# Optimization experiments

Hardware: AMD Instinct MI355X
Metric: run time of the kernel (lower is better)

## Reference

```python
import jax, jax.numpy as jnp
import numpy as np

N, D, O, H, T, S, R, BN = 4096, 256, 256, 256, 512, 8, 4, 2  # nodes, in, out, hidden, text_len, adj_size, relations used, basis_num


def setup_inputs() -> dict:
    key = jax.random.key(0)
    ks = jax.random.split(key, 16)
    sc = 0.05
    return {
        "entity_embeddings": jax.random.normal(ks[0], (N, D), jnp.float32) * sc,
        "text_encodings": jax.random.normal(ks[1], (1, T, 2 * H), jnp.float32) * sc,
        "adj_to_use": jnp.arange(R, dtype=jnp.int32),
        "adj_masks": jax.random.randint(ks[2], (R, N, N), 0, 2, dtype=jnp.int32),
        "text_guids": jax.random.normal(ks[3], (S, 2 * H), jnp.float32) * sc,
        "graph_guids_1": jax.random.normal(ks[4], (S, D), jnp.float32) * sc,
        "graph_guids_2": jax.random.normal(ks[5], (S, D), jnp.float32) * sc,
        "guid_a": jax.random.normal(ks[6], (S,), jnp.float32),
        "basis_V": jax.random.normal(ks[7], (D, BN, O), jnp.float32) * sc,
        "basis_b": jax.random.normal(ks[8], (S, BN), jnp.float32) * sc,
        "W_1": jax.random.normal(ks[9], (2 * H, D), jnp.float32) * sc,
        "W_2": jax.random.normal(ks[10], (2 * H, D), jnp.float32) * sc,
        "ln_gamma": jnp.ones((O,), jnp.float32),
        "ln_beta": jnp.zeros((O,), jnp.float32),
    }


def reference(entity_embeddings, text_encodings, adj_to_use, adj_masks,
              text_guids, graph_guids_1, graph_guids_2, guid_a,
              basis_V, basis_b, W_1, W_2, ln_gamma, ln_beta):
    te = text_encodings[0]                                  # [T, 2H] (batch of 1)
    tg = text_guids[adj_to_use]                             # [R, 2H]
    # text attention: softmax over T, per relation
    att = jax.nn.softmax(te @ tg.T, axis=0)                 # [T, R]
    context = att.T @ te                                    # [R, 2H]
    c1 = context @ W_1                                      # [R, D]
    c2 = context @ W_2
    ga = jax.nn.sigmoid(guid_a[adj_to_use])[:, None]        # [R, 1]
    g1 = ga * graph_guids_1[adj_to_use] + (1.0 - ga) * c1   # [R, D]
    g2 = ga * graph_guids_2[adj_to_use] + (1.0 - ga) * c2
    s1 = entity_embeddings @ g1.T                           # [N, R]
    s2 = entity_embeddings @ g2.T
    # A[r,i,j] = s1[i,r] + s2[j,r], masked softmax over j
    A = s1.T[:, :, None] + s2.T[:, None, :]                 # [R, N, N]
    A = jnp.where(adj_masks == 1, A, jnp.float32(-1e10))
    A = jax.nn.softmax(A, axis=-1)
    fused = jnp.einsum('rij,jd->rid', A, entity_embeddings) # [R, N, D]
    # torch.cat over relations on last dim -> column index r*D + d
    fused_cat = jnp.transpose(fused, (1, 0, 2)).reshape(N, R * D)
    # torch.matmul([R,BN],[D,BN,O]) -> [D,R,O], then .view(R*D, O) (row index d*R + r)
    bb = basis_b[adj_to_use]                                # [R, BN]
    W = jnp.einsum('rb,dbo->dro', bb, basis_V).reshape(D * R, O)
    out = fused_cat @ W                                     # [N, O]
    mu = jnp.mean(out, axis=-1, keepdims=True)
    var = jnp.var(out, axis=-1, keepdims=True)
    out = (out - mu) / jnp.sqrt(var + 1e-5) * ln_gamma + ln_beta
    return jax.nn.relu(out)
```

## Files before the change

kernel.cpp:

```cpp
#include <hip/hip_runtime.h>
#include <hip/hip_bf16.h>


typedef unsigned short u16;
typedef short bf16x8 __attribute__((ext_vector_type(8)));
typedef float f32x4 __attribute__((ext_vector_type(4)));
typedef int   v4i   __attribute__((ext_vector_type(4)));
typedef unsigned int v2u __attribute__((ext_vector_type(2)));

#define G2_OFF    0
#define E2_OFF    4096
#define WRT_OFF   69632
#define FPT_OFF   593920
#define FUSED_OFF 9506816
#define CAN_OFF   26284032

#define C_ENT 0
#define C_TE  1048576
#define C_TG  1310720
#define C_GG2 1314816
#define C_GA  1316864
#define C_BV  1316872
#define C_BB  1447944
#define C_W2  1447960
#define C_GAM 1579032
#define C_BET 1579288

__device__ __forceinline__ float b2f(u16 u) {
    union { unsigned int i; float f; } v; v.i = ((unsigned int)u) << 16; return v.f;
}
__device__ __forceinline__ u16 f2b(float f) {
    union { float f; unsigned int i; } v; v.f = f;
    return (u16)((v.i + 0x7FFFu + ((v.i >> 16) & 1u)) >> 16);
}

__global__ __launch_bounds__(256) void k_cvt(
    const void* s0, const void* s1, const void* s2, const void* s3,
    const void* s4, const void* s5, const void* s6, const void* s7,
    const void* s8, const void* s9, const unsigned* __restrict__ graw,
    u16* __restrict__ dst)
{
    bool isbf = (graw[0] == 0x3F803F80u);
    const void* srcs[10] = {s0, s1, s2, s3, s4, s5, s6, s7, s8, s9};
    const int ns[10]     = {1048576, 262144, 4096, 2048, 8, 131072, 16, 131072, 256, 256};
    const int offs[10]   = {C_ENT, C_TE, C_TG, C_GG2, C_GA, C_BV, C_BB, C_W2, C_GAM, C_BET};
    const int bstart[11] = {0, 512, 640, 642, 643, 644, 708, 709, 773, 774, 775};
    int b = blockIdx.x, a = 0;
    while (b >= bstart[a + 1]) ++a;
    int rel = b - bstart[a];
    int n = ns[a];
    u16* d = dst + offs[a];
    int base = rel * 2048 + threadIdx.x;
    if (isbf) {
        const u16* s = (const u16*)srcs[a];
        for (int k = 0; k < 8; ++k) { int i = base + k * 256; if (i < n) d[i] = s[i]; }
    } else {
        const float* s = (const float*)srcs[a];
        for (int k = 0; k < 8; ++k) { int i = base + k * 256; if (i < n) d[i] = f2b(s[i]); }
    }
}

__global__ __launch_bounds__(1024) void k_pre(const u16* __restrict__ te,
                                              const int* __restrict__ adj,
                                              const u16* __restrict__ tguids,
                                              const u16* __restrict__ gg2,
                                              const u16* __restrict__ guida,
                                              const u16* __restrict__ W2,
                                              float* __restrict__ g2ws) {
    __shared__ float s_tg[4 * 512];
    __shared__ float s_att[512 * 4];
    __shared__ float s_red[512 * 4];
    __shared__ float s_ctx[4 * 512];
    __shared__ float s_part[1024 * 4];
    int tid = threadIdx.x;
    int a[4] = {adj[0], adj[1], adj[2], adj[3]};
    for (int idx = tid; idx < 2048; idx += 1024) {
        int r = idx >> 9, h = idx & 511;
        s_tg[r * 512 + h] = b2f(tguids[a[r] * 512 + h]);
    }
    __syncthreads();
    {
        int t = tid & 511, half = tid >> 9;
        int h0 = half * 256;
        float s0 = 0.f, s1 = 0.f, s2 = 0.f, s3 = 0.f;
        const u16* row = te + t * 512 + h0;
        for (int hb = 0; hb < 256; hb += 8) {
            bf16x8 v = *(const bf16x8*)(row + hb);
            #pragma unroll
            for (int k = 0; k < 8; ++k) {
                float tv = b2f((u16)v[k]);
                int h = h0 + hb + k;
                s0 += tv * s_tg[h];        s1 += tv * s_tg[512 + h];
                s2 += tv * s_tg[1024 + h]; s3 += tv * s_tg[1536 + h];
            }
        }
        s_part[tid * 4 + 0] = s0; s_part[tid * 4 + 1] = s1;
        s_part[tid * 4 + 2] = s2; s_part[tid * 4 + 3] = s3;
    }
    __syncthreads();
    if (tid < 512) {
        for (int r = 0; r < 4; ++r) {
            float s = s_part[tid * 4 + r] + s_part[(512 + tid) * 4 + r];
            s_att[tid * 4 + r] = s; s_red[tid * 4 + r] = s;
        }
    }
    __syncthreads();
    for (int st = 256; st > 0; st >>= 1) {
        if (tid < st) for (int r = 0; r < 4; ++r)
            s_red[tid * 4 + r] = fmaxf(s_red[tid * 4 + r], s_red[(tid + st) * 4 + r]);
        __syncthreads();
    }
    float mx[4]; for (int r = 0; r < 4; ++r) mx[r] = s_red[r];
    __syncthreads();
    if (tid < 512) for (int r = 0; r < 4; ++r) {
        float e = __expf(s_att[tid * 4 + r] - mx[r]);
        s_att[tid * 4 + r] = e; s_red[tid * 4 + r] = e;
    }
    __syncthreads();
    for (int st = 256; st > 0; st >>= 1) {
        if (tid < st) for (int r = 0; r < 4; ++r)
            s_red[tid * 4 + r] += s_red[(tid + st) * 4 + r];
        __syncthreads();
    }
    float dn[4]; for (int r = 0; r < 4; ++r) dn[r] = s_red[r];
    __syncthreads();
    if (tid < 512) for (int r = 0; r < 4; ++r) s_att[tid * 4 + r] /= dn[r];
    __syncthreads();
    {
        int u = tid >> 2, tq = tid & 3;
        int r = u >> 6, h0 = (u & 63) * 8;
        float acc[8] = {};
        int t0 = tq * 128;
        for (int t = t0; t < t0 + 128; ++t) {
            bf16x8 v = *(const bf16x8*)(te + t * 512 + h0);
            float at = s_att[t * 4 + r];
            #pragma unroll
            for (int k = 0; k < 8; ++k) acc[k] += at * b2f((u16)v[k]);
        }
        #pragma unroll
        for (int k = 0; k < 8; ++k) {
            acc[k] += __shfl_xor(acc[k], 1);
            acc[k] += __shfl_xor(acc[k], 2);
        }
        if (tq == 0) {
            #pragma unroll
            for (int k = 0; k < 8; ++k) s_ctx[r * 512 + h0 + k] = acc[k];
        }
    }
    __syncthreads();
    {
        int r = tid >> 8, d = tid & 255;
        float acc = 0.f;
        for (int h = 0; h < 512; ++h) acc += s_ctx[r * 512 + h] * b2f(W2[h * 256 + d]);
        float gav = 1.f / (1.f + expf(-b2f(guida[a[r]])));
        g2ws[r * 256 + d] = gav * b2f(gg2[a[r] * 256 + d]) + (1.f - gav) * acc;
    }
}

__global__ __launch_bounds__(256) void k_s2_wrt(const u16* __restrict__ entity,
                                                const int* __restrict__ adj,
                                                const u16* __restrict__ basisV,
                                                const u16* __restrict__ basisb,
                                                const float* __restrict__ g2ws,
                                                float* __restrict__ e2ws,
                                                u16* __restrict__ wrt) {
    int b = blockIdx.x, tid = threadIdx.x;
    if (b < 16) {
        __shared__ float sg2[1024];
        for (int i = tid; i < 1024; i += 256) sg2[i] = g2ws[i];
        __syncthreads();
        int j = b * 256 + tid;
        const u16* erow = entity + j * 256;
        float a0 = 0.f, a1 = 0.f, a2 = 0.f, a3 = 0.f;
        for (int d0 = 0; d0 < 256; d0 += 8) {
            bf16x8 v = *(const bf16x8*)(erow + d0);
            #pragma unroll
            for (int k = 0; k < 8; ++k) {
                float ev = b2f((u16)v[k]);
                a0 += ev * sg2[d0 + k];       a1 += ev * sg2[256 + d0 + k];
                a2 += ev * sg2[512 + d0 + k]; a3 += ev * sg2[768 + d0 + k];
            }
        }
        e2ws[j] = expf(a0); e2ws[4096 + j] = expf(a1);
        e2ws[8192 + j] = expf(a2); e2ws[12288 + j] = expf(a3);
    } else {
        int b2 = b - 16; int r = b2 >> 6;
        int c = (b2 & 63) * 4 + (tid >> 6);
        int dq = tid & 63;
        int dbase = dq * 4;
        int a[4] = {adj[0], adj[1], adj[2], adj[3]};
        for (int dd = 0; dd < 4; ++dd) {
            float w = 0.f;
            for (int bi = 0; bi < 2; ++bi)
                w += b2f(basisb[a[dd] * 2 + bi]) * b2f(basisV[((64 * r + dq) * 2 + bi) * 256 + c]);
            wrt[(r * 256 + c) * 256 + dbase + dd] = f2b(w);
        }
    }
}

__global__ __launch_bounds__(256) void k_fplus(const u16* __restrict__ entity,
                                               const u16* __restrict__ wrt,
                                               const float* __restrict__ e2ws,
                                               u16* __restrict__ fpt) {
    int b = blockIdx.x, tid = threadIdx.x;
    if (b < 256) {
        int r = b & 3, ct = (b >> 2) & 3, jt = b >> 4;
        int c0 = ct * 64, j0 = jt * 256;
        __shared__ __align__(16) u16 lw[64 * 264];
        const u16* wr = wrt + (r * 256 + c0) * 256;
        for (int k = 0; k < 8; ++k) {
            int ci = tid + k * 256; int row = ci >> 5, off = (ci & 31) * 8;
            *(v4i*)(&lw[row * 264 + off]) = *(const v4i*)(wr + row * 256 + off);
        }
        __syncthreads();
        int wave = tid >> 6, ln = tid & 15, q = (tid & 63) >> 4;
        f32x4 acc[4][4] = {};
        for (int ks = 0; ks < 8; ++ks) {
            bf16x8 afr[4], bfr[4];
            for (int mt = 0; mt < 4; ++mt)
                afr[mt] = *(const bf16x8*)(&lw[(mt * 16 + ln) * 264 + ks * 32 + q * 8]);
            for (int nt = 0; nt < 4; ++nt) {
                int j = j0 + (wave * 4 + nt) * 16 + ln;
                bfr[nt] = *(const bf16x8*)(entity + j * 256 + ks * 32 + q * 8);
            }
            for (int mt = 0; mt < 4; ++mt)
                for (int nt = 0; nt < 4; ++nt)
                    acc[mt][nt] = __builtin_amdgcn_mfma_f32_16x16x32_bf16(afr[mt], bfr[nt], acc[mt][nt], 0, 0, 0);
        }
        for (int nt = 0; nt < 4; ++nt) {
            int j = j0 + (wave * 4 + nt) * 16 + ln;
            float e2j = e2ws[r * 4096 + j];
            int kt = j >> 5, kk = j & 31;
            u16* dst = fpt + (((size_t)(r * 128 + kt)) * 272 << 5);
            for (int mt = 0; mt < 4; ++mt)
                for (int reg = 0; reg < 4; ++reg) {
                    int c = c0 + mt * 16 + q * 4 + reg;
                    dst[(c << 5) + kk] = f2b(acc[mt][nt][reg] * e2j);
                }
        }
    } else {
        int b2 = b - 256; int r = b2 >> 1, half = b2 & 1;
        const float* e2r = e2ws + r * 4096;
        for (int it = 0; it < 128; ++it) {
            int l = it * 256 + tid;
            int kk = l & 31;
            int c  = 256 + ((l >> 5) & 15);
            int kt = half * 64 + (l >> 9);
            fpt[(((size_t)(r * 128 + kt) * 272 + c) << 5) + kk] =
                (c == 256) ? f2b(e2r[kt * 32 + kk]) : (u16)0;
        }
    }
}

__global__ __launch_bounds__(512) void k_big(const int* __restrict__ masks,
                                             const u16* __restrict__ fpt,
                                             float* __restrict__ fused) {
    __shared__ __align__(16) u16 lf[2][272 * 40];
    __shared__ float lden[64];
    int b = blockIdx.x, tid = threadIdx.x;
    int xcd = b & 7; int r = xcd & 3;
    int it = (b >> 3) + ((xcd >> 2) << 5);
    long i0 = (long)it * 64;
    const int* mbase = masks + ((long)r << 24) + i0 * 4096;
    const u16* fbase = fpt + (size_t)r * 128 * 272 * 32;
    int wave = tid >> 6, lane = tid & 63, ln = lane & 15, q = lane >> 4;
    int mg = wave >> 2, ng = wave & 3;
    const int* mr0 = mbase + (mg * 32 + ln) * 4096 + q * 8;
    const int* mr1 = mr0 + 16 * 4096;

    f32x4 acc[2][4] = {};
    f32x4 accD0 = {}, accD1 = {};

    struct Slot { v4i f0, f1, f2, m00, m01, m10, m11; };
    Slot s0, s1, s2, s3;
    auto load_slot = [&](int kt, Slot& s) {
        const u16* su = fbase + (size_t)kt * 8704;
        s.f0 = *(const v4i*)(su + tid * 8);
        s.f1 = *(const v4i*)(su + (tid + 512) * 8);
        if (tid < 64) s.f2 = *(const v4i*)(su + (tid + 1024) * 8);
        const int* p0 = mr0 + kt * 32;
        const int* p1 = mr1 + kt * 32;
        s.m00 = *(const v4i*)(p0);
        s.m01 = *(const v4i*)(p0 + 4);
        s.m10 = *(const v4i*)(p1);
        s.m11 = *(const v4i*)(p1 + 4);
    };
    auto cvt2 = [&](v4i lo, v4i hi) -> bf16x8 {
        v4i w;
        w.x = (int)((((unsigned)lo.x) | (((unsigned)lo.y) << 16)) * 0x3F80u);
        w.y = (int)((((unsigned)lo.z) | (((unsigned)lo.w) << 16)) * 0x3F80u);
        w.z = (int)((((unsigned)hi.x) | (((unsigned)hi.y) << 16)) * 0x3F80u);
        w.w = (int)((((unsigned)hi.z) | (((unsigned)hi.w) << 16)) * 0x3F80u);
        union { v4i i; bf16x8 h; } u; u.i = w; return u.h;
    };
    auto stage = [&](int par, const Slot& s) {
        u16* dst = &lf[par][0];
        *(v4i*)(dst + (tid >> 2) * 40 + (tid & 3) * 8) = s.f0;
        { int ci = tid + 512; *(v4i*)(dst + (ci >> 2) * 40 + (ci & 3) * 8) = s.f1; }
        if (tid < 64) { int ci = tid + 1024; *(v4i*)(dst + (ci >> 2) * 40 + (ci & 3) * 8) = s.f2; }
    };
    auto step = [&](int k, Slot& sM, Slot& sF) {
        if (k + 1 < 128) stage((k + 1) & 1, sF);
        bf16x8 a0 = cvt2(sM.m00, sM.m01);
        bf16x8 a1 = cvt2(sM.m10, sM.m11);
        if (k + 4 < 128) load_slot(k + 4, sM);
        const u16* src = &lf[k & 1][0];
        #pragma unroll
        for (int nt = 0; nt < 4; ++nt) {
            bf16x8 bf = *(const bf16x8*)(src + ((ng * 4 + nt) * 16 + ln) * 40 + q * 8);
            acc[0][nt] = __builtin_amdgcn_mfma_f32_16x16x32_bf16(a0, bf, acc[0][nt], 0, 0, 0);
            acc[1][nt] = __builtin_amdgcn_mfma_f32_16x16x32_bf16(a1, bf, acc[1][nt], 0, 0, 0);
        }
        if (ng == 3) {
            bf16x8 bf = *(const bf16x8*)(src + (256 + ln) * 40 + q * 8);
            accD0 = __builtin_amdgcn_mfma_f32_16x16x32_bf16(a0, bf, accD0, 0, 0, 0);
            accD1 = __builtin_amdgcn_mfma_f32_16x16x32_bf16(a1, bf, accD1, 0, 0, 0);
        }
        __syncthreads();
    };

    load_slot(0, s0);
    load_slot(1, s1);
    load_slot(2, s2);
    load_slot(3, s3);
    stage(0, s0);
    __syncthreads();
    #pragma unroll 1
    for (int kt = 0; kt < 128; kt += 4) {
        step(kt,     s0, s1);
        step(kt + 1, s1, s2);
        step(kt + 2, s2, s3);
        step(kt + 3, s3, s0);
    }

    if (ng == 3 && ln == 0) {
        #pragma unroll
        for (int reg = 0; reg < 4; ++reg) {
            lden[mg * 32 + q * 4 + reg]      = accD0[reg];
            lden[mg * 32 + 16 + q * 4 + reg] = accD1[reg];
        }
    }
    __syncthreads();
    float* fb = fused + ((long)r * 4096 + i0) * 256;
    #pragma unroll
    for (int mt = 0; mt < 2; ++mt) {
        float rd[4];
        #pragma unroll
        for (int reg = 0; reg < 4; ++reg) rd[reg] = 1.0f / lden[mg * 32 + mt * 16 + q * 4 + reg];
        #pragma unroll
        for (int nt = 0; nt < 4; ++nt) {
            int c = (ng * 4 + nt) * 16 + ln;
            #pragma unroll
            for (int reg = 0; reg < 4; ++reg) {
                int row = mg * 32 + mt * 16 + q * 4 + reg;
                __builtin_nontemporal_store(acc[mt][nt][reg] * rd[reg], fb + row * 256 + c);
            }
        }
    }
}

__global__ __launch_bounds__(256) void k_ln(const float* __restrict__ fused,
                                            const u16* __restrict__ gamma,
                                            const u16* __restrict__ beta,
                                            const unsigned* __restrict__ graw,
                                            void* __restrict__ outraw) {
    __shared__ float part[8];
    int i = blockIdx.x, o = threadIdx.x;
    float x = 0.f;
    for (int r = 0; r < 4; ++r)
        x += __builtin_nontemporal_load(fused + ((long)(r << 12) + i) * 256 + o);
    float s = x;
    #pragma unroll
    for (int st = 32; st > 0; st >>= 1) s += __shfl_xor(s, st);
    int w = o >> 6;
    if ((o & 63) == 0) part[w] = s;
    __syncthreads();
    float mu = (part[0] + part[1] + part[2] + part[3]) * (1.f / 256.f);
    float v = x - mu;
    float qv = v * v;
    #pragma unroll
    for (int st = 32; st > 0; st >>= 1) qv += __shfl_xor(qv, st);
    if ((o & 63) == 0) part[4 + w] = qv;
    __syncthreads();
    float var = (part[4] + part[5] + part[6] + part[7]) * (1.f / 256.f);
    float y = v * rsqrtf(var + 1e-5f) * b2f(gamma[o]) + b2f(beta[o]);
    float res = fmaxf(y, 0.f);
    bool isbf = (graw[0] == 0x3F803F80u);
    if (isbf) ((u16*)outraw)[i * 256 + o] = f2b(res);
    else      ((float*)outraw)[i * 256 + o] = res;
}

extern "C" void kernel_launch(void* const* d_in, const int* in_sizes, int n_in,
                              void* d_out, int out_size, void* d_ws, size_t ws_size,
                              hipStream_t stream) {
    const int* adj   = (const int*)d_in[2];
    const int* masks = (const int*)d_in[3];
    const unsigned* graw = (const unsigned*)d_in[12];
    char* ws = (char*)d_ws;
    float* g2ws = (float*)(ws + G2_OFF);
    float* e2ws = (float*)(ws + E2_OFF);
    u16*   wrt  = (u16*)(ws + WRT_OFF);
    u16*   fpt  = (u16*)(ws + FPT_OFF);
    float* fus  = (float*)(ws + FUSED_OFF);
    u16*   can  = (u16*)(ws + CAN_OFF);

    k_cvt<<<775, 256, 0, stream>>>(d_in[0], d_in[1], d_in[4], d_in[6], d_in[7],
                                   d_in[8], d_in[9], d_in[11], d_in[12], d_in[13],
                                   graw, can);
    const u16* entity = can + C_ENT;
    const u16* te     = can + C_TE;
    const u16* tguids = can + C_TG;
    const u16* gg2    = can + C_GG2;
    const u16* guida  = can + C_GA;
    const u16* basisV = can + C_BV;
    const u16* basisb = can + C_BB;
    const u16* W2     = can + C_W2;
    const u16* gamma  = can + C_GAM;
    const u16* beta   = can + C_BET;

    k_pre<<<1, 1024, 0, stream>>>(te, adj, tguids, gg2, guida, W2, g2ws);
    k_s2_wrt<<<272, 256, 0, stream>>>(entity, adj, basisV, basisb, g2ws, e2ws, wrt);
    k_fplus<<<264, 256, 0, stream>>>(entity, wrt, e2ws, fpt);
    k_big<<<256, 512, 0, stream>>>(masks, fpt, fus);
    k_ln<<<4096, 256, 0, stream>>>(fus, gamma, beta, graw, d_out);
}
```

Before: 577.0 us.

## Stage adjacency masks through LDS with one nontemporal load per thread

The mask tile is no longer loaded redundantly per wave in MFMA fragment layout. Each thread now loads one 16-byte chunk with a nontemporal load, converts it to bf16, and writes it into a double-buffered LDS tile that waves read as A fragments. This removes the duplicated global mask reads across the four N-group waves and cuts per-thread register use for prefetch slots. The cost is extra LDS traffic and shared memory.

```diff
diff --git a/kernel.cpp b/kernel.cpp
--- a/kernel.cpp
+++ b/kernel.cpp
@@ -255,6 +255,7 @@
 __global__ __launch_bounds__(512) void k_big(const int* __restrict__ masks,
                                              const u16* __restrict__ fpt,
                                              float* __restrict__ fused) {
+    __shared__ __align__(16) u16 lm[2][64 * 40];
     __shared__ __align__(16) u16 lf[2][272 * 40];
     __shared__ float lden[64];
     int b = blockIdx.x, tid = threadIdx.x;
@@ -263,48 +264,41 @@
     long i0 = (long)it * 64;
     const int* mbase = masks + ((long)r << 24) + i0 * 4096;
     const u16* fbase = fpt + (size_t)r * 128 * 272 * 32;
+    int mrow = tid >> 3, mch = tid & 7;
     int wave = tid >> 6, lane = tid & 63, ln = lane & 15, q = lane >> 4;
     int mg = wave >> 2, ng = wave & 3;
-    const int* mr0 = mbase + (mg * 32 + ln) * 4096 + q * 8;
-    const int* mr1 = mr0 + 16 * 4096;
 
     f32x4 acc[2][4] = {};
     f32x4 accD0 = {}, accD1 = {};
 
-    struct Slot { v4i f0, f1, f2, m00, m01, m10, m11; };
+    struct Slot { v4i pm, f0, f1, f2; };
     Slot s0, s1, s2, s3;
     auto load_slot = [&](int kt, Slot& s) {
+        s.pm = __builtin_nontemporal_load((const v4i*)(mbase + mrow * 4096 + kt * 32 + mch * 4));
         const u16* su = fbase + (size_t)kt * 8704;
         s.f0 = *(const v4i*)(su + tid * 8);
         s.f1 = *(const v4i*)(su + (tid + 512) * 8);
         if (tid < 64) s.f2 = *(const v4i*)(su + (tid + 1024) * 8);
-        const int* p0 = mr0 + kt * 32;
-        const int* p1 = mr1 + kt * 32;
-        s.m00 = *(const v4i*)(p0);
-        s.m01 = *(const v4i*)(p0 + 4);
-        s.m10 = *(const v4i*)(p1);
-        s.m11 = *(const v4i*)(p1 + 4);
-    };
-    auto cvt2 = [&](v4i lo, v4i hi) -> bf16x8 {
-        v4i w;
-        w.x = (int)((((unsigned)lo.x) | (((unsigned)lo.y) << 16)) * 0x3F80u);
-        w.y = (int)((((unsigned)lo.z) | (((unsigned)lo.w) << 16)) * 0x3F80u);
-        w.z = (int)((((unsigned)hi.x) | (((unsigned)hi.y) << 16)) * 0x3F80u);
-        w.w = (int)((((unsigned)hi.z) | (((unsigned)hi.w) << 16)) * 0x3F80u);
-        union { v4i i; bf16x8 h; } u; u.i = w; return u.h;
     };
     auto stage = [&](int par, const Slot& s) {
+        {
+            unsigned m0 = (unsigned)s.pm.x * 0x3F80u, m1 = (unsigned)s.pm.y * 0x3F80u;
+            unsigned m2 = (unsigned)s.pm.z * 0x3F80u, m3 = (unsigned)s.pm.w * 0x3F80u;
+            v2u w; w.x = m0 | (m1 << 16); w.y = m2 | (m3 << 16);
+            *(v2u*)(&lm[par][mrow * 40 + mch * 4]) = w;
+        }
         u16* dst = &lf[par][0];
         *(v4i*)(dst + (tid >> 2) * 40 + (tid & 3) * 8) = s.f0;
         { int ci = tid + 512; *(v4i*)(dst + (ci >> 2) * 40 + (ci & 3) * 8) = s.f1; }
         if (tid < 64) { int ci = tid + 1024; *(v4i*)(dst + (ci >> 2) * 40 + (ci & 3) * 8) = s.f2; }
     };
     auto step = [&](int k, Slot& sM, Slot& sF) {
+        const u16* msrc = &lm[k & 1][0];
+        const u16* src  = &lf[k & 1][0];
+        bf16x8 a0 = *(const bf16x8*)(msrc + (mg * 32 + ln) * 40 + q * 8);
+        bf16x8 a1 = *(const bf16x8*)(msrc + (mg * 32 + 16 + ln) * 40 + q * 8);
         if (k + 1 < 128) stage((k + 1) & 1, sF);
-        bf16x8 a0 = cvt2(sM.m00, sM.m01);
-        bf16x8 a1 = cvt2(sM.m10, sM.m11);
         if (k + 4 < 128) load_slot(k + 4, sM);
-        const u16* src = &lf[k & 1][0];
         #pragma unroll
         for (int nt = 0; nt < 4; ++nt) {
             bf16x8 bf = *(const bf16x8*)(src + ((ng * 4 + nt) * 16 + ln) * 40 + q * 8);
```

New measurement: 545.5 us. 1.06x faster.
